# Kernel tuning notes

Hardware: AMD Instinct MI355X
Metric: run time of the kernel (lower is better)

## Reference

```python
import jax, jax.numpy as jnp
import numpy as np
import math

N_, LQ, C = 8, 300, 256
HEADS, NLVL, NPTS = 8, 4, 8
D_HEAD = C // HEADS
LEVELS = [(128, 128), (64, 64), (32, 32), (16, 16)]
LEN_IN = sum(h * w for h, w in LEVELS)
STARTS = np.cumsum([0] + [h * w for h, w in LEVELS])
MH, MW = 128, 128  # reference mask resolution


def _offset_bias():
    # replicates _reset_parameters grid init for sampling_offsets.bias
    thetas = np.arange(HEADS, dtype=np.float32) * (2.0 * math.pi / HEADS)
    grid = np.stack([np.cos(thetas), np.sin(thetas)], -1)  # (H, 2)
    grid = grid / np.abs(grid).max(-1, keepdims=True)
    grid = np.tile(grid[:, None, None, :], (1, NLVL, NPTS, 1))  # (H, L, P, 2)
    for i in range(NPTS):
        grid[:, :, i, :] *= i + 1
    return jnp.asarray(grid.reshape(-1), dtype=jnp.float32)


def setup_inputs() -> dict:
    key = jax.random.key(0)
    ks = jax.random.split(key, 8)
    query = jax.random.normal(ks[0], (N_, LQ, C), dtype=jnp.float32)
    reference_bboxs = jax.random.normal(ks[1], (N_, LQ, 4), dtype=jnp.float32)
    reference_masks = jax.random.normal(ks[2], (N_, LQ, MH, MW), dtype=jnp.float32)
    input_flatten = jax.random.normal(ks[3], (N_, LEN_IN, C), dtype=jnp.float32)
    input_spatial_shapes = jnp.asarray(LEVELS, dtype=jnp.int64)
    input_level_start_index = jnp.asarray(STARTS[:-1], dtype=jnp.int64)
    input_padding_mask = jnp.zeros((N_, LEN_IN), dtype=bool)
    s = 1.0 / math.sqrt(C)
    W_off = jax.random.normal(ks[4], (C, HEADS * NLVL * NPTS * 2), dtype=jnp.float32) * 0.01
    b_off = _offset_bias()
    W_attn = jax.random.normal(ks[5], (C, HEADS * NLVL * NPTS), dtype=jnp.float32) * 0.01
    b_attn = jnp.zeros((HEADS * NLVL * NPTS,), dtype=jnp.float32)
    W_val = jax.random.normal(ks[6], (C, C), dtype=jnp.float32) * s
    b_val = jnp.zeros((C,), dtype=jnp.float32)
    W_out = jax.random.normal(ks[7], (C, C), dtype=jnp.float32) * s
    b_out = jnp.zeros((C,), dtype=jnp.float32)
    return dict(query=query, reference_bboxs=reference_bboxs, reference_masks=reference_masks,
                mask_threshold=0, input_flatten=input_flatten,
                input_spatial_shapes=input_spatial_shapes,
                input_level_start_index=input_level_start_index,
                input_padding_mask=input_padding_mask,
                W_off=W_off, b_off=b_off, W_attn=W_attn, b_attn=b_attn,
                W_val=W_val, b_val=b_val, W_out=W_out, b_out=b_out)


def get_bounding_boxes(masks):
    # masks: (N, Q, H, W) bool -> normalized (cx, cy, w, h), (N, Q, 4)
    H, W = masks.shape[-2:]
    xs = masks.any(-2)  # (N, Q, W)
    ys = masks.any(-1)  # (N, Q, H)
    xi = jnp.arange(W, dtype=jnp.float32)
    yi = jnp.arange(H, dtype=jnp.float32)
    x_min = jnp.min(jnp.where(xs, xi, float(W)), -1)
    x_max = jnp.max(jnp.where(xs, xi, -1.0), -1)
    y_min = jnp.min(jnp.where(ys, yi, float(H)), -1)
    y_max = jnp.max(jnp.where(ys, yi, -1.0), -1)
    nonempty = xs.any(-1)
    x0, x1 = x_min / W, (x_max + 1.0) / W
    y0, y1 = y_min / H, (y_max + 1.0) / H
    box = jnp.stack([(x0 + x1) * 0.5, (y0 + y1) * 0.5, x1 - x0, y1 - y0], -1)
    return jnp.where(nonempty[..., None], box, 0.0)


def check_points_in_mask(mask, points):
    # mask: (N, Q, H, W) bool; points: (N, Q, P, 2) normalized -> (N, Q, P) float
    N, Q, H, W = mask.shape
    px = jnp.clip((points[..., 0] * W).astype(jnp.int32), 0, W - 1)
    py = jnp.clip((points[..., 1] * H).astype(jnp.int32), 0, H - 1)
    idx = py * W + px  # (N, Q, P)
    flat = mask.reshape(N, Q, H * W)
    return jnp.take_along_axis(flat, idx, axis=2).astype(jnp.float32)


def ms_deform_attn_core(value, sampling_locations, attention_weights):
    # value: (N, Len_in, heads, d); loc: (N, Lq, heads, L, P, 2); w: (N, Lq, heads, L, P)
    N, Lq = sampling_locations.shape[:2]
    out = jnp.zeros((N, Lq, HEADS, D_HEAD), dtype=value.dtype)
    for l, (Hl, Wl) in enumerate(LEVELS):
        v = value[:, STARTS[l]:STARTS[l + 1]].transpose(0, 2, 1, 3)  # (N, heads, Hl*Wl, d)
        loc = sampling_locations[:, :, :, l]  # (N, Lq, heads, P, 2)
        # grid_sample(align_corners=False): pixel = loc*size - 0.5
        px = loc[..., 0] * Wl - 0.5
        py = loc[..., 1] * Hl - 0.5
        x0 = jnp.floor(px); y0 = jnp.floor(py)
        wx1 = px - x0; wy1 = py - y0
        x0i = x0.astype(jnp.int32); y0i = y0.astype(jnp.int32)

        def gather(xi, yi):
            valid = (xi >= 0) & (xi < Wl) & (yi >= 0) & (yi < Hl)
            idx = jnp.clip(yi, 0, Hl - 1) * Wl + jnp.clip(xi, 0, Wl - 1)  # (N, Lq, heads, P)
            idx2 = idx.transpose(0, 2, 1, 3).reshape(N, HEADS, Lq * NPTS)
            g = jnp.take_along_axis(v, idx2[..., None], axis=2)  # (N, heads, Lq*P, d)
            g = g.reshape(N, HEADS, Lq, NPTS, D_HEAD).transpose(0, 2, 1, 3, 4)
            return g * valid[..., None].astype(g.dtype)

        samp = (gather(x0i, y0i) * ((1 - wx1) * (1 - wy1))[..., None]
                + gather(x0i + 1, y0i) * (wx1 * (1 - wy1))[..., None]
                + gather(x0i, y0i + 1) * ((1 - wx1) * wy1)[..., None]
                + gather(x0i + 1, y0i + 1) * (wx1 * wy1)[..., None])
        out = out + jnp.einsum('nqhpd,nqhp->nqhd', samp, attention_weights[:, :, :, l])
    return out.reshape(N, Lq, C)


def reference(query, reference_bboxs, reference_masks, mask_threshold, input_flatten,
              input_spatial_shapes, input_level_start_index, input_padding_mask,
              W_off, b_off, W_attn, b_attn, W_val, b_val, W_out, b_out):
    N, Lq, _ = query.shape
    value = input_flatten @ W_val + b_val
    value = jnp.where(input_padding_mask[..., None], 0.0, value)
    value = value.reshape(N, LEN_IN, HEADS, D_HEAD)
    offsets = (query @ W_off + b_off).reshape(N, Lq, HEADS, NLVL, NPTS, 2)
    attw = (query @ W_attn + b_attn).reshape(N, Lq, HEADS, NLVL, NPTS)
    ref_masks = reference_masks > 0
    box = get_bounding_boxes(ref_masks)  # (N, Lq, 4) normalized cxcywh
    ctr = box[:, :, None, None, None, :2]
    wh = box[:, :, None, None, None, 2:]
    loc = ctr + offsets / NPTS * wh * 0.5  # (N, Lq, heads, L, P, 2)
    pin = check_points_in_mask(ref_masks, loc.reshape(N, Lq, -1, 2))
    attw = attw * pin.reshape(N, Lq, HEADS, NLVL, NPTS)
    attw = jax.nn.softmax(attw.reshape(N, Lq, HEADS, NLVL * NPTS), -1)
    attw = attw.reshape(N, Lq, HEADS, NLVL, NPTS)
    out = ms_deform_attn_core(value, loc, attw)
    return out @ W_out + b_out
```

## Files before the change

kernel.cpp:

```cpp
#include <hip/hip_runtime.h>
#include <math.h>

#define NB    8
#define LQ    300
#define CC    256
#define HEADS 8
#define NLVL  4
#define NPTS  8
#define DH    32
#define LEN_IN 21760
#define NQ    (NB*LQ)
#define MH    128
#define MW    128

typedef __attribute__((ext_vector_type(8))) short bf16x8;
typedef __attribute__((ext_vector_type(8))) unsigned short ushort8;
typedef __attribute__((ext_vector_type(4))) float f32x4;
typedef unsigned short ushort;
typedef unsigned int uint;

#define AS1 __attribute__((address_space(1)))
#define AS3 __attribute__((address_space(3)))

static __device__ __forceinline__ ushort f2bf(float f) {
    uint u = __builtin_bit_cast(uint, f);
    uint r = (u + 0x7fffu + ((u >> 16) & 1u)) >> 16;
    return (ushort)r;
}
static __device__ __forceinline__ float bf2f(ushort u) {
    return __builtin_bit_cast(float, ((uint)u) << 16);
}

__global__ void transpose_cast_w(const float* __restrict__ W, ushort* __restrict__ Bt) {
    int n = blockIdx.x, k = threadIdx.x;
    Bt[n * CC + k] = f2bf(W[(size_t)k * CC + n]);
}

__global__ __launch_bounds__(256) void gemm_mfma_value(
    const float* __restrict__ A, const ushort* __restrict__ Bt,
    const float* __restrict__ bias, ushort* __restrict__ C, int M)
{
    __shared__ ushort As[128 * 32];
    __shared__ ushort Bs[128 * 32];
    const int tid  = threadIdx.x;
    const int wave = tid >> 6, lane = tid & 63;
    const int bm = blockIdx.x * 128;
    const int bn = blockIdx.y * 128;
    const int wm = (wave >> 1) * 64, wn = (wave & 1) * 64;

    f32x4 acc[4][4] = {};

    const int am = tid >> 1, ak = (tid & 1) * 16;
    const float* aptr = A + (size_t)(bm + am) * CC + ak;
    ushort* as_dst = &As[am * 32 + ak];
    AS3 char* bs_base = (AS3 char*)Bs;
    const int fr = lane & 15, kg = lane >> 4;

    for (int kt = 0; kt < 8; ++kt) {
        const float* ap = aptr + kt * 32;
        float4 f0 = *(const float4*)(ap + 0);
        float4 f1 = *(const float4*)(ap + 4);
        float4 f2 = *(const float4*)(ap + 8);
        float4 f3 = *(const float4*)(ap + 12);
        ushort8 u0, u1;
        u0[0]=f2bf(f0.x); u0[1]=f2bf(f0.y); u0[2]=f2bf(f0.z); u0[3]=f2bf(f0.w);
        u0[4]=f2bf(f1.x); u0[5]=f2bf(f1.y); u0[6]=f2bf(f1.z); u0[7]=f2bf(f1.w);
        u1[0]=f2bf(f2.x); u1[1]=f2bf(f2.y); u1[2]=f2bf(f2.z); u1[3]=f2bf(f2.w);
        u1[4]=f2bf(f3.x); u1[5]=f2bf(f3.y); u1[6]=f2bf(f3.z); u1[7]=f2bf(f3.w);
        *(ushort8*)(as_dst + 0) = u0;
        *(ushort8*)(as_dst + 8) = u1;
        #pragma unroll
        for (int j = 0; j < 2; ++j) {
            int c = wave * 128 + j * 64 + lane;
            const ushort* g = Bt + (size_t)(bn + (c >> 2)) * CC + kt * 32 + (c & 3) * 8;
            __builtin_amdgcn_global_load_lds((const AS1 void*)g,
                                             (AS3 void*)(bs_base + (wave * 128 + j * 64) * 16),
                                             16, 0, 0);
        }
        __syncthreads();
        bf16x8 af[4], bfv[4];
        #pragma unroll
        for (int i = 0; i < 4; ++i)
            af[i] = *(const bf16x8*)&As[(wm + i * 16 + fr) * 32 + kg * 8];
        #pragma unroll
        for (int j = 0; j < 4; ++j)
            bfv[j] = *(const bf16x8*)&Bs[(wn + j * 16 + fr) * 32 + kg * 8];
        #pragma unroll
        for (int i = 0; i < 4; ++i)
            #pragma unroll
            for (int j = 0; j < 4; ++j)
                acc[i][j] = __builtin_amdgcn_mfma_f32_16x16x32_bf16(af[i], bfv[j], acc[i][j], 0, 0, 0);
        __syncthreads();
    }

    const int col0 = lane & 15, rq = (lane >> 4) * 4;
    #pragma unroll
    for (int j = 0; j < 4; ++j) {
        const int col = bn + wn + j * 16 + col0;
        const float bv = bias[col];
        #pragma unroll
        for (int i = 0; i < 4; ++i) {
            const int row = bm + wm + i * 16 + rq;
            #pragma unroll
            for (int r = 0; r < 4; ++r)
                C[(size_t)(row + r) * CC + col] = f2bf(acc[i][j][r] + bv);
        }
    }
}

#define TM 64
#define TN 64
#define TK 16

__global__ __launch_bounds__(256) void gemm_bias_kernel(
    const float* __restrict__ A, const float* __restrict__ B,
    const float* __restrict__ bias, float* __restrict__ Cmat,
    int M, int N, int K)
{
    __shared__ float As[TK][TM + 4];
    __shared__ float Bs[TK][TN + 4];
    const int tid = threadIdx.x;
    const int bm = blockIdx.x * TM;
    const int bn = blockIdx.y * TN;
    const int tm = (tid >> 4) << 2;
    const int tn = (tid & 15) << 2;
    float acc[4][4] = {};

    for (int k0 = 0; k0 < K; k0 += TK) {
        #pragma unroll
        for (int i = 0; i < 4; ++i) {
            int idx = tid + i * 256;
            int m = idx >> 4;
            int k = idx & 15;
            int gm = bm + m;
            float v = 0.f;
            if (gm < M) v = A[(size_t)gm * K + k0 + k];
            As[k][m] = v;
        }
        #pragma unroll
        for (int i = 0; i < 4; ++i) {
            int idx = tid + i * 256;
            int k = idx >> 6;
            int n = idx & 63;
            int gn = bn + n;
            float v = 0.f;
            if (gn < N) v = B[(size_t)(k0 + k) * N + gn];
            Bs[k][n] = v;
        }
        __syncthreads();
        #pragma unroll
        for (int k = 0; k < TK; ++k) {
            float a[4], b[4];
            #pragma unroll
            for (int i = 0; i < 4; ++i) a[i] = As[k][tm + i];
            #pragma unroll
            for (int j = 0; j < 4; ++j) b[j] = Bs[k][tn + j];
            #pragma unroll
            for (int i = 0; i < 4; ++i)
                #pragma unroll
                for (int j = 0; j < 4; ++j)
                    acc[i][j] = fmaf(a[i], b[j], acc[i][j]);
        }
        __syncthreads();
    }

    #pragma unroll
    for (int i = 0; i < 4; ++i) {
        int m = bm + tm + i;
        if (m >= M) continue;
        #pragma unroll
        for (int j = 0; j < 4; ++j) {
            int n = bn + tn + j;
            if (n < N) Cmat[(size_t)m * N + n] = acc[i][j] + bias[n];
        }
    }
}

__global__ __launch_bounds__(256) void bbox_kernel(
    const float* __restrict__ masks, float* __restrict__ boxes)
{
    const int b   = blockIdx.x;
    const int tid = threadIdx.x;
    const float4* m4 = (const float4*)(masks + (size_t)b * (MH * MW));

    int wmin = MW, wmax = -1, hmin = MH, hmax = -1;
    #pragma unroll
    for (int it = 0; it < 16; ++it) {
        int i = tid + it * 256;
        float4 v = m4[i];
        int base = i << 2;
        int h = base >> 7;
        int w0 = base & 127;
        bool a0 = v.x > 0.f, a1 = v.y > 0.f, a2 = v.z > 0.f, a3 = v.w > 0.f;
        if (a0 | a1 | a2 | a3) { hmin = min(hmin, h); hmax = max(hmax, h); }
        if (a0) { wmin = min(wmin, w0);     wmax = max(wmax, w0);     }
        if (a1) { wmin = min(wmin, w0 + 1); wmax = max(wmax, w0 + 1); }
        if (a2) { wmin = min(wmin, w0 + 2); wmax = max(wmax, w0 + 2); }
        if (a3) { wmin = min(wmin, w0 + 3); wmax = max(wmax, w0 + 3); }
    }
    #pragma unroll
    for (int off = 32; off; off >>= 1) {
        wmin = min(wmin, __shfl_xor(wmin, off));
        wmax = max(wmax, __shfl_xor(wmax, off));
        hmin = min(hmin, __shfl_xor(hmin, off));
        hmax = max(hmax, __shfl_xor(hmax, off));
    }
    __shared__ int s_wmin[4], s_wmax[4], s_hmin[4], s_hmax[4];
    const int wave = tid >> 6;
    if ((tid & 63) == 0) {
        s_wmin[wave] = wmin; s_wmax[wave] = wmax;
        s_hmin[wave] = hmin; s_hmax[wave] = hmax;
    }
    __syncthreads();
    if (tid == 0) {
        int a = MW, bx = -1, c = MH, d = -1;
        #pragma unroll
        for (int i = 0; i < 4; ++i) {
            a = min(a, s_wmin[i]); bx = max(bx, s_wmax[i]);
            c = min(c, s_hmin[i]); d = max(d, s_hmax[i]);
        }
        float4 box;
        if (bx >= 0) {
            float x0 = a * (1.f / MW), x1 = (bx + 1) * (1.f / MW);
            float y0 = c * (1.f / MH), y1 = (d + 1) * (1.f / MH);
            box = make_float4((x0 + x1) * 0.5f, (y0 + y1) * 0.5f, x1 - x0, y1 - y0);
        } else {
            box = make_float4(0.f, 0.f, 0.f, 0.f);
        }
        *(float4*)(boxes + (size_t)b * 4) = box;
    }
}

template<int WL>
static __device__ __forceinline__ float sample_level(
    const ushort* __restrict__ vbase, int st,
    const float* __restrict__ s_lx, const float* __restrict__ s_ly,
    const float* __restrict__ s_w, int ptbase)
{
    float acc = 0.f;
    #pragma unroll
    for (int p = 0; p < NPTS; ++p) {
        const int pt = ptbase + p;
        const float fx = s_lx[pt] * WL - 0.5f;
        const float fy = s_ly[pt] * WL - 0.5f;
        const float pw = s_w[pt];
        const float x0f = floorf(fx), y0f = floorf(fy);
        const float wx = fx - x0f, wy = fy - y0f;
        const int x0 = (int)x0f, y0 = (int)y0f;
        const int x1 = x0 + 1, y1 = y0 + 1;
        const int x0c = min(max(x0, 0), WL - 1);
        const int x1c = min(max(x1, 0), WL - 1);
        const int y0c = min(max(y0, 0), WL - 1);
        const int y1c = min(max(y1, 0), WL - 1);
        const float vx0 = (x0 >= 0 && x0 < WL) ? 1.f : 0.f;
        const float vx1 = (x1 >= 0 && x1 < WL) ? 1.f : 0.f;
        const float vy0 = (y0 >= 0 && y0 < WL) ? 1.f : 0.f;
        const float vy1 = (y1 >= 0 && y1 < WL) ? 1.f : 0.f;
        const ushort* r0 = vbase + (size_t)(st + y0c * WL) * CC;
        const ushort* r1 = vbase + (size_t)(st + y1c * WL) * CC;
        const float v00 = bf2f(r0[(size_t)x0c * CC]);
        const float v01 = bf2f(r0[(size_t)x1c * CC]);
        const float v10 = bf2f(r1[(size_t)x0c * CC]);
        const float v11 = bf2f(r1[(size_t)x1c * CC]);
        const float w00 = vx0 * vy0 * (1.f - wx) * (1.f - wy);
        const float w01 = vx1 * vy0 * wx * (1.f - wy);
        const float w10 = vx0 * vy1 * (1.f - wx) * wy;
        const float w11 = vx1 * vy1 * wx * wy;
        acc += pw * (w00 * v00 + w01 * v01 + w10 * v10 + w11 * v11);
    }
    return acc;
}

__global__ __launch_bounds__(512) void sample_kernel(
    const float* __restrict__ masks,
    const ushort* __restrict__ value,
    const float* __restrict__ offs,
    const float* __restrict__ attw,
    const float* __restrict__ boxes,
    float* __restrict__ samp)
{
    const int b   = blockIdx.x;
    const int n   = b / LQ;
    const int tid = threadIdx.x;

    __shared__ float s_lx[256], s_ly[256], s_w[256], s_acc[256];

    if (tid < 256) {
        const float4 box = *(const float4*)(boxes + (size_t)b * 4);
        const float ox = offs[(size_t)b * 512 + tid * 2 + 0];
        const float oy = offs[(size_t)b * 512 + tid * 2 + 1];
        const float lx = box.x + ox * (1.f / NPTS) * box.z * 0.5f;
        const float ly = box.y + oy * (1.f / NPTS) * box.w * 0.5f;
        int px = (int)(lx * MW); px = min(max(px, 0), MW - 1);
        int py = (int)(ly * MH); py = min(max(py, 0), MH - 1);
        const float pin = (masks[(size_t)b * (MH * MW) + py * MW + px] > 0.f) ? 1.f : 0.f;
        const float logit = attw[(size_t)b * 256 + tid] * pin;
        float mx = logit;
        #pragma unroll
        for (int off = 16; off; off >>= 1) mx = fmaxf(mx, __shfl_xor(mx, off, 32));
        const float e = expf(logit - mx);
        float ssum = e;
        #pragma unroll
        for (int off = 16; off; off >>= 1) ssum += __shfl_xor(ssum, off, 32);
        s_lx[tid] = lx; s_ly[tid] = ly; s_w[tid] = e / ssum;
    }
    __syncthreads();

    const int half = tid >> 8;
    const int h = (tid >> 5) & 7, d = tid & 31;
    const ushort* vbase = value + (size_t)n * LEN_IN * CC + h * DH + d;
    float acc;
    if (half == 0) {
        acc  = sample_level<128>(vbase, 0,     s_lx, s_ly, s_w, (h * NLVL + 0) * NPTS);
        acc += sample_level< 64>(vbase, 16384, s_lx, s_ly, s_w, (h * NLVL + 1) * NPTS);
        s_acc[tid] = acc;
    } else {
        acc  = sample_level< 32>(vbase, 20480, s_lx, s_ly, s_w, (h * NLVL + 2) * NPTS);
        acc += sample_level< 16>(vbase, 21504, s_lx, s_ly, s_w, (h * NLVL + 3) * NPTS);
    }
    __syncthreads();
    if (half == 1)
        samp[(size_t)b * 256 + (tid - 256)] = acc + s_acc[tid - 256];
}

extern "C" void kernel_launch(void* const* d_in, const int* in_sizes, int n_in,
                              void* d_out, int out_size, void* d_ws, size_t ws_size,
                              hipStream_t stream)
{
    const float* query  = (const float*)d_in[0];
    const float* masks  = (const float*)d_in[2];
    const float* flat   = (const float*)d_in[4];
    const float* W_off  = (const float*)d_in[8];
    const float* b_off  = (const float*)d_in[9];
    const float* W_attn = (const float*)d_in[10];
    const float* b_attn = (const float*)d_in[11];
    const float* W_val  = (const float*)d_in[12];
    const float* b_val  = (const float*)d_in[13];
    const float* W_out  = (const float*)d_in[14];
    const float* b_out  = (const float*)d_in[15];
    float* out = (float*)d_out;

    float*  offs  = (float*)d_ws;
    float*  attw  = offs + (size_t)NQ * 512;
    float*  samp  = attw + (size_t)NQ * 256;
    float*  boxes = samp + (size_t)NQ * 256;
    ushort* value = (ushort*)(boxes + (size_t)NQ * 4);
    ushort* Bt    = value + (size_t)NB * LEN_IN * CC;

    const int Mval = NB * LEN_IN;

    transpose_cast_w<<<CC, CC, 0, stream>>>(W_val, Bt);
    gemm_mfma_value<<<dim3(Mval / 128, CC / 128), 256, 0, stream>>>(
        flat, Bt, b_val, value, Mval);
    gemm_bias_kernel<<<dim3((NQ + TM - 1) / TM, 512 / TN), 256, 0, stream>>>(
        query, W_off, b_off, offs, NQ, 512, CC);
    gemm_bias_kernel<<<dim3((NQ + TM - 1) / TM, CC / TN), 256, 0, stream>>>(
        query, W_attn, b_attn, attw, NQ, CC, CC);
    bbox_kernel<<<NQ, 256, 0, stream>>>(masks, boxes);
    sample_kernel<<<NQ, 512, 0, stream>>>(masks, value, offs, attw, boxes, samp);
    gemm_bias_kernel<<<dim3((NQ + TM - 1) / TM, CC / TN), 256, 0, stream>>>(
        samp, W_out, b_out, out, NQ, CC, CC);
}
```

Baseline: 582.3 us.

## Preload full swizzled B panel in LDS and stream A fragments from registers

The value-projection GEMM now loads the block's whole 128x256 bf16 weight panel into LDS once, using an XOR swizzle to avoid bank conflicts. Each wave reads its A fragments straight from global memory into registers and prefetches the next k-step, so the per-iteration barriers and the A staging through LDS go away. The cost is 64KB of LDS per block, which lowers occupancy, plus duplicated A global loads across the two waves that share rows.

```diff
diff --git a/kernel.cpp b/kernel.cpp
--- a/kernel.cpp
+++ b/kernel.cpp
@@ -36,61 +36,74 @@
     Bt[n * CC + k] = f2bf(W[(size_t)k * CC + n]);
 }
 
+#define BSWZ(r, cb) (((r) << 9) + ((cb) ^ (((r) & 7) << 4)))
+
 __global__ __launch_bounds__(256) void gemm_mfma_value(
     const float* __restrict__ A, const ushort* __restrict__ Bt,
     const float* __restrict__ bias, ushort* __restrict__ C, int M)
 {
-    __shared__ ushort As[128 * 32];
-    __shared__ ushort Bs[128 * 32];
+    __shared__ ushort Bs[128 * 256];
+    char* bs = (char*)Bs;
     const int tid  = threadIdx.x;
     const int wave = tid >> 6, lane = tid & 63;
     const int bm = blockIdx.x * 128;
     const int bn = blockIdx.y * 128;
     const int wm = (wave >> 1) * 64, wn = (wave & 1) * 64;
 
+    #pragma unroll
+    for (int it = 0; it < 16; ++it) {
+        int idx = it * 256 + tid;
+        int r   = idx >> 5;
+        int c8  = idx & 31;
+        ushort8 v = *(const ushort8*)(Bt + (size_t)(bn + r) * CC + c8 * 8);
+        *(ushort8*)(bs + BSWZ(r, c8 * 16)) = v;
+    }
+    __syncthreads();
+
     f32x4 acc[4][4] = {};
-
-    const int am = tid >> 1, ak = (tid & 1) * 16;
-    const float* aptr = A + (size_t)(bm + am) * CC + ak;
-    ushort* as_dst = &As[am * 32 + ak];
-    AS3 char* bs_base = (AS3 char*)Bs;
     const int fr = lane & 15, kg = lane >> 4;
-
+    const float* aA = A + (size_t)(bm + wm + fr) * CC + kg * 8;
+
+    float4 fA[4][2];
+    #pragma unroll
+    for (int i = 0; i < 4; ++i) {
+        const float* ap = aA + (size_t)(i * 16) * CC;
+        fA[i][0] = *(const float4*)(ap);
+        fA[i][1] = *(const float4*)(ap + 4);
+    }
+
+    #pragma unroll
     for (int kt = 0; kt < 8; ++kt) {
-        const float* ap = aptr + kt * 32;
-        float4 f0 = *(const float4*)(ap + 0);
-        float4 f1 = *(const float4*)(ap + 4);
-        float4 f2 = *(const float4*)(ap + 8);
-        float4 f3 = *(const float4*)(ap + 12);
-        ushort8 u0, u1;
-        u0[0]=f2bf(f0.x); u0[1]=f2bf(f0.y); u0[2]=f2bf(f0.z); u0[3]=f2bf(f0.w);
-        u0[4]=f2bf(f1.x); u0[5]=f2bf(f1.y); u0[6]=f2bf(f1.z); u0[7]=f2bf(f1.w);
-        u1[0]=f2bf(f2.x); u1[1]=f2bf(f2.y); u1[2]=f2bf(f2.z); u1[3]=f2bf(f2.w);
-        u1[4]=f2bf(f3.x); u1[5]=f2bf(f3.y); u1[6]=f2bf(f3.z); u1[7]=f2bf(f3.w);
-        *(ushort8*)(as_dst + 0) = u0;
-        *(ushort8*)(as_dst + 8) = u1;
-        #pragma unroll
-        for (int j = 0; j < 2; ++j) {
-            int c = wave * 128 + j * 64 + lane;
-            const ushort* g = Bt + (size_t)(bn + (c >> 2)) * CC + kt * 32 + (c & 3) * 8;
-            __builtin_amdgcn_global_load_lds((const AS1 void*)g,
-                                             (AS3 void*)(bs_base + (wave * 128 + j * 64) * 16),
-                                             16, 0, 0);
-        }
-        __syncthreads();
-        bf16x8 af[4], bfv[4];
-        #pragma unroll
-        for (int i = 0; i < 4; ++i)
-            af[i] = *(const bf16x8*)&As[(wm + i * 16 + fr) * 32 + kg * 8];
+        bf16x8 bfv[4];
         #pragma unroll
         for (int j = 0; j < 4; ++j)
-            bfv[j] = *(const bf16x8*)&Bs[(wn + j * 16 + fr) * 32 + kg * 8];
+            bfv[j] = *(const bf16x8*)(bs + BSWZ(wn + j * 16 + fr, kt * 64 + kg * 16));
+
+        bf16x8 af[4];
+        #pragma unroll
+        for (int i = 0; i < 4; ++i) {
+            ushort8 u;
+            u[0] = f2bf(fA[i][0].x); u[1] = f2bf(fA[i][0].y);
+            u[2] = f2bf(fA[i][0].z); u[3] = f2bf(fA[i][0].w);
+            u[4] = f2bf(fA[i][1].x); u[5] = f2bf(fA[i][1].y);
+            u[6] = f2bf(fA[i][1].z); u[7] = f2bf(fA[i][1].w);
+            af[i] = __builtin_bit_cast(bf16x8, u);
+        }
+
+        if (kt < 7) {
+            #pragma unroll
+            for (int i = 0; i < 4; ++i) {
+                const float* ap = aA + (size_t)(i * 16) * CC + (kt + 1) * 32;
+                fA[i][0] = *(const float4*)(ap);
+                fA[i][1] = *(const float4*)(ap + 4);
+            }
+        }
+
         #pragma unroll
         for (int i = 0; i < 4; ++i)
             #pragma unroll
             for (int j = 0; j < 4; ++j)
                 acc[i][j] = __builtin_amdgcn_mfma_f32_16x16x32_bf16(af[i], bfv[j], acc[i][j], 0, 0, 0);
-        __syncthreads();
     }
 
     const int col0 = lane & 15, rq = (lane >> 4) * 4;
```

Result: slower. 611.1 us (+4.9%).
